# Optimization experiments

Measured on AMD Instinct MI355X. Metric: run time of the kernel, lower is better.

The kernel has to match this reference:

```python
import jax, jax.numpy as jnp
import numpy as np

# dims
B, S, D, H, DH, M, L, V, BS, NR = 4, 2048, 512, 8, 64, 2048, 6, 32000, 64, 3
NB = S // BS  # 32 blocks


def _block_plan(nb, seed):
    """BigBird block connectivity: 2 global + 3 window + NR random blocks per query block.
    Returns idx [nb, K] int32 and validity mask [nb, K] bool (dedup + edge handling)."""
    rng = np.random.RandomState(seed)
    K = 5 + NR
    idx = np.zeros((nb, K), np.int32)
    msk = np.zeros((nb, K), bool)
    for i in range(nb):
        fixed = {0, nb - 1} | {j for j in (i - 1, i, i + 1) if 0 <= j < nb}
        rest = [j for j in range(nb) if j not in fixed]
        rnd = rng.choice(rest, size=min(NR, len(rest)), replace=False) if rest else []
        sel = sorted(fixed | set(int(r) for r in rnd))
        idx[i, :len(sel)] = sel
        msk[i, :len(sel)] = True
    return jnp.asarray(idx), jnp.asarray(msk)


def _posemb():
    pos = np.arange(S, dtype=np.float32)[:, None]
    div = np.exp(np.arange(0, D, 2, dtype=np.float32) * (-np.log(10000.0) / D))
    pe = np.zeros((S, D), np.float32)
    pe[:, 0::2] = np.sin(pos * div)
    pe[:, 1::2] = np.cos(pos * div)
    return jnp.asarray(pe)


def _ln(x, scale, bias):
    m = jnp.mean(x, axis=-1, keepdims=True)
    v = jnp.mean(jnp.square(x - m), axis=-1, keepdims=True)
    return (x - m) * jax.lax.rsqrt(v + 1e-6) * scale + bias


def _bigbird_attn(x, key_mask, wq, wk, wv, wo, idx, bmask):
    # x: [B,S,D]; idx/bmask: [NB,K]
    q = jnp.einsum('bsd,dhe->bshe', x, wq).reshape(B, NB, BS, H, DH)
    k = jnp.einsum('bsd,dhe->bshe', x, wk).reshape(B, NB, BS, H, DH)
    v = jnp.einsum('bsd,dhe->bshe', x, wv).reshape(B, NB, BS, H, DH)
    kg = k[:, idx]  # [B,NB,K,BS,H,DH] gathered key blocks
    vg = v[:, idx]
    scores = jnp.einsum('bnqhe,bnkche->bhnqkc', q, kg) / jnp.sqrt(jnp.float32(DH))
    kmb = key_mask.reshape(B, NB, BS)[:, idx]          # [B,NB,K,BS]
    m = kmb & bmask[None, :, :, None]                   # [B,NB,K,BS]
    scores = jnp.where(m[:, None, :, None, :, :], scores, jnp.float32(-1e9))
    Kc = idx.shape[1]
    attn = jax.nn.softmax(scores.reshape(B, H, NB, BS, Kc * BS), axis=-1)
    attn = attn.reshape(B, H, NB, BS, Kc, BS)
    out = jnp.einsum('bhnqkc,bnkche->bnqhe', attn, vg).reshape(B, S, H, DH)
    return jnp.einsum('bshe,hed->bsd', out, wo)


def setup_inputs() -> dict:
    key = jax.random.key(0)
    ks = jax.random.split(key, 12)
    n = jax.random.normal
    inp = {
        'tokens': jax.random.randint(ks[0], (B, S), 0, V, dtype=jnp.int32),
        'embed': n(ks[1], (V, D), dtype=jnp.float32),
        'ln1_s': jnp.ones((L, D), jnp.float32), 'ln1_b': jnp.zeros((L, D), jnp.float32),
        'wq': n(ks[2], (L, D, H, DH), dtype=jnp.float32) * 0.02,
        'wk': n(ks[3], (L, D, H, DH), dtype=jnp.float32) * 0.02,
        'wv': n(ks[4], (L, D, H, DH), dtype=jnp.float32) * 0.02,
        'wo': n(ks[5], (L, H, DH, D), dtype=jnp.float32) * 0.02,
        'ln2_s': jnp.ones((L, D), jnp.float32), 'ln2_b': jnp.zeros((L, D), jnp.float32),
        'w1': n(ks[6], (L, D, M), dtype=jnp.float32) * 0.02, 'b1': jnp.zeros((L, M), jnp.float32),
        'w2': n(ks[7], (L, M, D), dtype=jnp.float32) * 0.02, 'b2': jnp.zeros((L, D), jnp.float32),
        'lnf_s': jnp.ones((D,), jnp.float32), 'lnf_b': jnp.zeros((D,), jnp.float32),
    }
    return inp


def reference(tokens, embed, ln1_s, ln1_b, wq, wk, wv, wo, ln2_s, ln2_b, w1, b1, w2, b2, lnf_s, lnf_b):
    key_mask = tokens > 0                      # src padding mask
    x = embed[tokens] + _posemb()[None]        # [B,S,D]
    plans = [_block_plan(NB, l) for l in range(L)]  # connectivity_seed = layer index
    for l in range(L):
        idx, bm = plans[l]
        h = _ln(x, ln1_s[l], ln1_b[l])
        x = x + _bigbird_attn(h, key_mask, wq[l], wk[l], wv[l], wo[l], idx, bm)
        y = _ln(x, ln2_s[l], ln2_b[l])
        y = jax.nn.gelu(jnp.einsum('bsd,dm->bsm', y, w1[l]) + b1[l])
        y = jnp.einsum('bsm,md->bsd', y, w2[l]) + b2[l]
        x = x + y
    return _ln(x, lnf_s, lnf_b)
```

## Files before the change

### kernel.cpp

```cpp
#include <hip/hip_runtime.h>

using u32 = unsigned int;
using u16 = unsigned short;

#define B_   4
#define S_   2048
#define D_   512
#define H_   8
#define DH_  64
#define FF_  2048
#define L_   6
#define NB_  32
#define KC_  8

typedef __attribute__((ext_vector_type(8))) __bf16 bf16x8;
typedef __attribute__((ext_vector_type(4))) float  f32x4;

struct Plan { unsigned char idx[NB_][KC_]; unsigned char cnt[NB_]; };

#define QSCALE 0.18033688011112042f

__device__ __forceinline__ u16 f2b(float f) {
  union { __bf16 b; u16 u; } x;
  x.b = (__bf16)f;
  return x.u;
}

__device__ __forceinline__ float gelu_f(float x) {
  float y2 = 1.5957691216f * x + 0.0713548163f * x * x * x;
  return x / (1.0f + __expf(-y2));
}

typedef const __attribute__((address_space(1))) u32* gas_t;
typedef __attribute__((address_space(3))) u32* las_t;
__device__ __forceinline__ void glds16(const u16* g, u16* l) {
  __builtin_amdgcn_global_load_lds((gas_t)g, (las_t)l, 16, 0, 0);
}

__global__ __launch_bounds__(256)
void transpose_conv(const float* __restrict__ in, u16* __restrict__ out, int R, int C,
                    size_t lstride, int rowoff) {
  __shared__ float tile[32][33];
  const int l = blockIdx.z;
  const float* src = in + (size_t)l * R * C;
  u16* dst = out + (size_t)l * lstride;
  const int c0 = blockIdx.x * 32, r0 = blockIdx.y * 32;
  const int tx = threadIdx.x, ty = threadIdx.y;
#pragma unroll
  for (int i = 0; i < 4; i++)
    tile[ty + i * 8][tx] = src[(size_t)(r0 + ty + i * 8) * C + c0 + tx];
  __syncthreads();
#pragma unroll
  for (int i = 0; i < 4; i++)
    dst[(size_t)(rowoff + c0 + ty + i * 8) * R + r0 + tx] = f2b(tile[tx][ty + i * 8]);
}

__global__ __launch_bounds__(128)
void embed_kernel(const int* __restrict__ tokens, const float* __restrict__ emb,
                  float* __restrict__ x) {
  const int row = blockIdx.x;
  const int s = row & (S_ - 1);
  const int t = threadIdx.x;
  const int tok = tokens[row];
  float4 v = ((const float4*)(emb + (size_t)tok * D_))[t];
  float va[4] = {v.x, v.y, v.z, v.w};
  const float cc = -2.0f * logf(10000.0f) / (float)D_;
  const float pos = (float)s;
#pragma unroll
  for (int j = 0; j < 4; j++) {
    int d = t * 4 + j;
    int i = d >> 1;
    float dv = expf(cc * (float)i);
    float ang = pos * dv;
    va[j] += (d & 1) ? cosf(ang) : sinf(ang);
  }
  ((float4*)x)[(size_t)row * (D_ / 4) + t] = make_float4(va[0], va[1], va[2], va[3]);
}

template <bool BF16OUT>
__global__ __launch_bounds__(128)
void ln_kernel(const float* __restrict__ x, const float* __restrict__ sc,
               const float* __restrict__ bi, void* __restrict__ outp) {
  const int row = blockIdx.x;
  const int t = threadIdx.x;
  float4 v = ((const float4*)(x + (size_t)row * D_))[t];
  float va[4] = {v.x, v.y, v.z, v.w};
  float s = va[0] + va[1] + va[2] + va[3];
  float sq = va[0] * va[0] + va[1] * va[1] + va[2] * va[2] + va[3] * va[3];
#pragma unroll
  for (int d = 1; d < 64; d <<= 1) {
    s  += __shfl_xor(s, d);
    sq += __shfl_xor(sq, d);
  }
  __shared__ float red[4];
  const int wv = t >> 6, lane = t & 63;
  if (lane == 0) { red[wv * 2] = s; red[wv * 2 + 1] = sq; }
  __syncthreads();
  const float ts  = red[0] + red[2];
  const float tsq = red[1] + red[3];
  const float mean = ts * (1.0f / (float)D_);
  const float inv  = rsqrtf(tsq * (1.0f / (float)D_) - mean * mean + 1e-6f);
  const int d0 = t * 4;
  float o[4];
#pragma unroll
  for (int j = 0; j < 4; j++)
    o[j] = (va[j] - mean) * inv * sc[d0 + j] + bi[d0 + j];
  if (BF16OUT) {
    ushort4 u;
    u.x = f2b(o[0]); u.y = f2b(o[1]); u.z = f2b(o[2]); u.w = f2b(o[3]);
    ((ushort4*)outp)[(size_t)row * (D_ / 4) + t] = u;
  } else {
    ((float4*)outp)[(size_t)row * (D_ / 4) + t] = make_float4(o[0], o[1], o[2], o[3]);
  }
}

template <int MODE, bool VSPLIT, int TM, int TN>
__global__ __launch_bounds__(TN * 2)
void gemm_pipe(const u16* __restrict__ A, const u16* __restrict__ BT,
               int Kk, int ostride, int ncols,
               float* __restrict__ outf, u16* __restrict__ outb,
               const float* __restrict__ bias, const float* __restrict__ resid,
               u16* __restrict__ vtout) {
  constexpr int NW  = TN / 32;
  constexpr int WC  = NW / 2;
  constexpr int MI  = TM / 32;
  constexpr int CHA = TM / (8 * NW);
  constexpr int CHB = TN / (8 * NW);
  constexpr int VM  = CHA + CHB;
  __shared__ u16 As[2][TM * 64];
  __shared__ u16 Bs[2][TN * 64];
  const int tid = threadIdx.x;
  const int wave = tid >> 6, lane = tid & 63;
  const int nwg = gridDim.x, cpx = nwg >> 3;
  const int bid = blockIdx.x;
  const int gid = (bid & 7) * cpx + (bid >> 3);
  const int row0 = (gid / ncols) * TM, col0 = (gid % ncols) * TN;
  const int wr = wave / WC, wc = wave % WC;
  const int l15 = lane & 15, l4 = lane >> 4;

  const u16* asrc[CHA];
  const u16* bsrc[CHB];
  int adst[CHA], bdst[CHB];
#pragma unroll
  for (int i = 0; i < CHA; i++) {
    int chunk = wave * (CHA * 64) + i * 64 + lane;
    int r = chunk >> 3, s = chunk & 7;
    asrc[i] = A + (size_t)(row0 + r) * Kk + ((s ^ (r & 7)) << 3);
    adst[i] = (wave * (CHA * 64) + i * 64) * 8;
  }
#pragma unroll
  for (int i = 0; i < CHB; i++) {
    int chunk = wave * (CHB * 64) + i * 64 + lane;
    int r = chunk >> 3, s = chunk & 7;
    bsrc[i] = BT + (size_t)(col0 + r) * Kk + ((s ^ (r & 7)) << 3);
    bdst[i] = (wave * (CHB * 64) + i * 64) * 8;
  }

  int aoff[MI], boff[4];
#pragma unroll
  for (int m = 0; m < MI; m++) aoff[m] = (wr * (MI * 16) + m * 16 + l15) * 64;
#pragma unroll
  for (int n = 0; n < 4; n++) boff[n] = (wc * 64 + n * 16 + l15) * 64;
  const int sk0 = ((l4)     ^ (l15 & 7)) << 3;
  const int sk1 = ((4 + l4) ^ (l15 & 7)) << 3;

  f32x4 acc[MI][4] = {};
  const int nk = Kk >> 6;

  auto stage = [&](int buf, int kt) {
    const int ko = kt << 6;
#pragma unroll
    for (int i = 0; i < CHA; i++) glds16(asrc[i] + ko, &As[buf][adst[i]]);
#pragma unroll
    for (int i = 0; i < CHB; i++) glds16(bsrc[i] + ko, &Bs[buf][bdst[i]]);
  };

  stage(0, 0);
  stage(1, 1);

  for (int kt = 0; kt < nk; ++kt) {
    const int cur = kt & 1;
    if (kt + 1 < nk) {
      if constexpr (VM == 8) { asm volatile("s_waitcnt vmcnt(8)" ::: "memory"); }
      else                   { asm volatile("s_waitcnt vmcnt(6)" ::: "memory"); }
    } else {
      asm volatile("s_waitcnt vmcnt(0)" ::: "memory");
    }
    __builtin_amdgcn_s_barrier();
    __builtin_amdgcn_sched_barrier(0);

    bf16x8 af0[MI], bf0[4];
#pragma unroll
    for (int m = 0; m < MI; m++) af0[m] = *(const bf16x8*)&As[cur][aoff[m] + sk0];
#pragma unroll
    for (int n = 0; n < 4; n++) bf0[n] = *(const bf16x8*)&Bs[cur][boff[n] + sk0];
#pragma unroll
    for (int m = 0; m < MI; m++)
#pragma unroll
      for (int n = 0; n < 4; n++)
        acc[m][n] = __builtin_amdgcn_mfma_f32_16x16x32_bf16(af0[m], bf0[n], acc[m][n], 0, 0, 0);

    bf16x8 af1[MI], bf1[4];
#pragma unroll
    for (int m = 0; m < MI; m++) af1[m] = *(const bf16x8*)&As[cur][aoff[m] + sk1];
#pragma unroll
    for (int n = 0; n < 4; n++) bf1[n] = *(const bf16x8*)&Bs[cur][boff[n] + sk1];
    asm volatile("s_waitcnt lgkmcnt(0)" ::: "memory");
    __builtin_amdgcn_sched_barrier(0);
    __builtin_amdgcn_s_barrier();
    __builtin_amdgcn_sched_barrier(0);
    if (kt + 2 < nk) stage(cur, kt + 2);

    __builtin_amdgcn_s_setprio(1);
#pragma unroll
    for (int m = 0; m < MI; m++)
#pragma unroll
      for (int n = 0; n < 4; n++)
        acc[m][n] = __builtin_amdgcn_mfma_f32_16x16x32_bf16(af1[m], bf1[n], acc[m][n], 0, 0, 0);
    __builtin_amdgcn_s_setprio(0);
  }

#pragma unroll
  for (int m = 0; m < MI; m++) {
#pragma unroll
    for (int n = 0; n < 4; n++) {
      const int c = col0 + wc * 64 + n * 16 + l15;
      const int rb = row0 + wr * (MI * 16) + m * 16 + l4 * 4;
      if (VSPLIT && c >= 1024) {
        u16 pk[4];
#pragma unroll
        for (int j = 0; j < 4; j++) pk[j] = f2b(acc[m][n][j]);
        *(uint2*)(vtout + (size_t)(c - 1024) * (B_ * S_) + rb) = *(const uint2*)pk;
      } else {
#pragma unroll
        for (int j = 0; j < 4; j++) {
          const size_t o = (size_t)(rb + j) * ostride + c;
          float v = acc[m][n][j];
          if (MODE == 0) {
            if (VSPLIT && c < 512) v *= QSCALE;
            outb[o] = f2b(v);
          } else if (MODE == 1) {
            outf[o] = v + resid[o];
          } else if (MODE == 2) {
            outb[o] = f2b(gelu_f(v + bias[c]));
          } else {
            outf[o] = v + bias[c] + resid[o];
          }
        }
      }
    }
  }
}

__global__ __launch_bounds__(256, 4)
void attn_mfma(const u16* __restrict__ qkv, const u16* __restrict__ vTg,
               const int* __restrict__ tokens, u16* __restrict__ outb, Plan plan) {
  __shared__ u16 ks[2][64 * 64];
  __shared__ u16 vt[2][64 * 64];
  __shared__ u16 ps[64 * 64];

  const int blk = blockIdx.x;
  const int h0 = blk & 7;
  const int n  = (blk >> 3) & 31;
  const int b  = blk >> 8;
  const int t  = threadIdx.x;
  const int wave = t >> 6, lane = t & 63;
  const int l15 = lane & 15, l4 = lane >> 4;
  const int ncnt = plan.cnt[n];
  const int qrow0 = b * S_ + n * 64;

  auto stage = [&](int bi, int c, int* tkd) {
    const int krow0 = b * S_ + c * 64;
#pragma unroll
    for (int i = 0; i < 2; i++) {
      int c0 = i * 256 + wave * 64;
      int cl = c0 + lane;
      int r = cl >> 3, s = cl & 7;
      int sw = (s ^ (r & 7)) << 3;
      glds16(qkv + (size_t)(krow0 + r) * 1024 + 512 + h0 * 64 + sw, &ks[bi][c0 * 8]);
      glds16(vTg + (size_t)(h0 * 64 + r) * (B_ * S_) + krow0 + sw, &vt[bi][c0 * 8]);
    }
#pragma unroll
    for (int nn = 0; nn < 4; nn++) tkd[nn] = tokens[krow0 + nn * 16 + l15];
  };

  bf16x8 qaf[2];
#pragma unroll
  for (int ks_ = 0; ks_ < 2; ks_++)
    qaf[ks_] = *(const bf16x8*)(qkv + (size_t)(qrow0 + wave * 16 + l15) * 1024 +
                                h0 * 64 + ks_ * 32 + l4 * 8);

  int tk[4], tn[4];
  stage(0, plan.idx[n][0], tk);

  f32x4 oacc[4] = {};
  float mrow[4], lrow[4];
#pragma unroll
  for (int j = 0; j < 4; j++) { mrow[j] = -3e38f; lrow[j] = 0.0f; }

  for (int kc = 0; kc < ncnt; kc++) {
    const int cur = kc & 1;
    __syncthreads();
    if (kc + 1 < ncnt) stage(cur ^ 1, plan.idx[n][kc + 1], tn);

    f32x4 sacc[4] = {};
#pragma unroll
    for (int nn = 0; nn < 4; nn++) {
      int r = nn * 16 + l15;
#pragma unroll
      for (int ks_ = 0; ks_ < 2; ks_++) {
        bf16x8 kf = *(const bf16x8*)(&ks[cur][r * 64 + ((ks_ * 32 + l4 * 8) ^ ((r & 7) << 3))]);
        sacc[nn] = __builtin_amdgcn_mfma_f32_16x16x32_bf16(qaf[ks_], kf, sacc[nn], 0, 0, 0);
      }
    }

    bool vld[4];
#pragma unroll
    for (int nn = 0; nn < 4; nn++) vld[nn] = tk[nn] > 0;

    float rmax[4];
#pragma unroll
    for (int j = 0; j < 4; j++) {
      float mj = -3e38f;
#pragma unroll
      for (int nn = 0; nn < 4; nn++)
        if (vld[nn]) mj = fmaxf(mj, sacc[nn][j]);
      rmax[j] = mj;
    }
#pragma unroll
    for (int d = 1; d < 16; d <<= 1) {
#pragma unroll
      for (int j = 0; j < 4; j++) rmax[j] = fmaxf(rmax[j], __shfl_xor(rmax[j], d));
    }
    int chg = 0;
#pragma unroll
    for (int j = 0; j < 4; j++) chg |= (rmax[j] > mrow[j]);
    if (__ballot(chg)) {
#pragma unroll
      for (int j = 0; j < 4; j++) {
        float mn = fmaxf(mrow[j], rmax[j]);
        float alpha = exp2f(mrow[j] - mn);
        mrow[j] = mn;
        lrow[j] *= alpha;
#pragma unroll
        for (int n2 = 0; n2 < 4; n2++) oacc[n2][j] *= alpha;
      }
    }
    float p[4][4];
#pragma unroll
    for (int j = 0; j < 4; j++) {
      float psum = 0.0f;
#pragma unroll
      for (int nn = 0; nn < 4; nn++) {
        float pv = vld[nn] ? exp2f(sacc[nn][j] - mrow[j]) : 0.0f;
        p[nn][j] = pv;
        psum += pv;
      }
      lrow[j] += psum;
    }

#pragma unroll
    for (int nn = 0; nn < 4; nn++)
#pragma unroll
      for (int j = 0; j < 4; j++) {
        int q = wave * 16 + l4 * 4 + j;
        ps[q * 64 + ((nn * 16 + l15) ^ ((q & 7) << 3))] = f2b(p[nn][j]);
      }

#pragma unroll
    for (int ks_ = 0; ks_ < 2; ks_++) {
      int r = wave * 16 + l15;
      bf16x8 paf = *(const bf16x8*)(ps + r * 64 + ((ks_ * 32 + l4 * 8) ^ ((r & 7) << 3)));
#pragma unroll
      for (int n2 = 0; n2 < 4; n2++) {
        int rv = n2 * 16 + l15;
        bf16x8 vf = *(const bf16x8*)(&vt[cur][rv * 64 + ((ks_ * 32 + l4 * 8) ^ ((rv & 7) << 3))]);
        oacc[n2] = __builtin_amdgcn_mfma_f32_16x16x32_bf16(paf, vf, oacc[n2], 0, 0, 0);
      }
    }
#pragma unroll
    for (int nn = 0; nn < 4; nn++) tk[nn] = tn[nn];
  }

#pragma unroll
  for (int d = 1; d < 16; d <<= 1) {
#pragma unroll
    for (int j = 0; j < 4; j++) lrow[j] += __shfl_xor(lrow[j], d);
  }
#pragma unroll
  for (int j = 0; j < 4; j++) {
    const float inv = lrow[j] > 0.0f ? 1.0f / lrow[j] : 0.0f;
    const int q = n * 64 + wave * 16 + l4 * 4 + j;
#pragma unroll
    for (int n2 = 0; n2 < 4; n2++) {
      outb[(size_t)(b * S_ + q) * D_ + h0 * 64 + n2 * 16 + l15] = f2b(oacc[n2][j] * inv);
    }
  }
}

namespace {
struct HostMT {
  u32 mt[624]; int mti;
  void seed(u32 s) {
    mt[0] = s;
    for (int i = 1; i < 624; i++)
      mt[i] = 1812433253u * (mt[i - 1] ^ (mt[i - 1] >> 30)) + (u32)i;
    mti = 624;
  }
  u32 next() {
    if (mti >= 624) {
      for (int k = 0; k < 624; k++) {
        u32 y = (mt[k] & 0x80000000u) | (mt[(k + 1) % 624] & 0x7fffffffu);
        mt[k] = mt[(k + 397) % 624] ^ (y >> 1) ^ ((y & 1u) ? 0x9908b0dfu : 0u);
      }
      mti = 0;
    }
    u32 y = mt[mti++];
    y ^= y >> 11;
    y ^= (y << 7)  & 0x9d2c5680u;
    y ^= (y << 15) & 0xefc60000u;
    y ^= y >> 18;
    return y;
  }
  u32 interval(u32 mx) {
    if (mx == 0u) return 0u;
    u32 mask = mx;
    mask |= mask >> 1; mask |= mask >> 2; mask |= mask >> 4;
    mask |= mask >> 8; mask |= mask >> 16;
    u32 v;
    while ((v = (next() & mask)) > mx) {}
    return v;
  }
};

void build_plan(int l, Plan* out) {
  HostMT rng;
  rng.seed((u32)l);
  for (int i = 0; i < NB_; i++) {
    bool fixedv[NB_] = {};
    fixedv[0] = true; fixedv[NB_ - 1] = true;
    for (int j = i - 1; j <= i + 1; j++)
      if (j >= 0 && j < NB_) fixedv[j] = true;
    int rest[NB_]; int nr = 0;
    for (int j = 0; j < NB_; j++) if (!fixedv[j]) rest[nr++] = j;
    int perm[NB_];
    for (int tt = 0; tt < nr; tt++) perm[tt] = tt;
    for (int tt = nr - 1; tt >= 1; tt--) {
      int j = (int)rng.interval((u32)tt);
      int tmp = perm[tt]; perm[tt] = perm[j]; perm[j] = tmp;
    }
    bool sel[NB_];
    for (int j = 0; j < NB_; j++) sel[j] = fixedv[j];
    for (int c = 0; c < 3; c++) sel[rest[perm[c]]] = true;
    int cnt = 0;
    for (int j = 0; j < NB_; j++)
      if (sel[j]) out->idx[i][cnt++] = (unsigned char)j;
    out->cnt[i] = (unsigned char)cnt;
    for (int c2 = cnt; c2 < KC_; c2++) out->idx[i][c2] = 0;
  }
}
}

extern "C" void kernel_launch(void* const* d_in, const int* in_sizes, int n_in,
                              void* d_out, int out_size, void* d_ws, size_t ws_size,
                              hipStream_t stream) {
  (void)in_sizes; (void)n_in; (void)out_size; (void)ws_size;

  const int*   tokens = (const int*)d_in[0];
  const float* embed  = (const float*)d_in[1];
  const float* ln1_s  = (const float*)d_in[2];
  const float* ln1_b  = (const float*)d_in[3];
  const float* wq     = (const float*)d_in[4];
  const float* wk     = (const float*)d_in[5];
  const float* wv     = (const float*)d_in[6];
  const float* wo     = (const float*)d_in[7];
  const float* ln2_s  = (const float*)d_in[8];
  const float* ln2_b  = (const float*)d_in[9];
  const float* w1     = (const float*)d_in[10];
  const float* b1     = (const float*)d_in[11];
  const float* w2     = (const float*)d_in[12];
  const float* b2     = (const float*)d_in[13];
  const float* lnf_s  = (const float*)d_in[14];
  const float* lnf_b  = (const float*)d_in[15];

  char* wp = (char*)d_ws;
  auto take = [&](size_t bytes) {
    void* p = (void*)wp;
    wp += (bytes + 255) & ~(size_t)255;
    return p;
  };

  const int Mrows = B_ * S_;
  u16* wqkvT = (u16*)take((size_t)L_ * 1536 * D_ * 2);
  u16* woT   = (u16*)take((size_t)L_ * D_ * D_ * 2);
  u16* w1T   = (u16*)take((size_t)L_ * FF_ * D_ * 2);
  u16* w2T   = (u16*)take((size_t)L_ * D_ * FF_ * 2);
  float* x   = (float*)take((size_t)Mrows * D_ * 4);
  u16* h     = (u16*)take((size_t)Mrows * D_ * 2);
  u16* big   = (u16*)take((size_t)Mrows * FF_ * 2);
  u16* qkv   = big;
  u16* vT    = big + (size_t)Mrows * 1024;
  u16* g     = big;

  Plan plans[L_];
  for (int l = 0; l < L_; l++) build_plan(l, &plans[l]);

  const size_t qkvL = (size_t)1536 * D_;

  transpose_conv<<<dim3(D_ / 32, D_ / 32, L_), dim3(32, 8), 0, stream>>>(wq, wqkvT, D_, D_, qkvL, 0);
  transpose_conv<<<dim3(D_ / 32, D_ / 32, L_), dim3(32, 8), 0, stream>>>(wk, wqkvT, D_, D_, qkvL, 512);
  transpose_conv<<<dim3(D_ / 32, D_ / 32, L_), dim3(32, 8), 0, stream>>>(wv, wqkvT, D_, D_, qkvL, 1024);
  transpose_conv<<<dim3(D_ / 32, D_ / 32, L_), dim3(32, 8), 0, stream>>>(wo, woT, D_, D_, (size_t)D_ * D_, 0);
  transpose_conv<<<dim3(FF_ / 32, D_ / 32, L_), dim3(32, 8), 0, stream>>>(w1, w1T, D_, FF_, (size_t)FF_ * D_, 0);
  transpose_conv<<<dim3(D_ / 32, FF_ / 32, L_), dim3(32, 8), 0, stream>>>(w2, w2T, FF_, D_, (size_t)D_ * FF_, 0);
  embed_kernel<<<Mrows, 128, 0, stream>>>(tokens, embed, x);

  for (int l = 0; l < L_; l++) {
    ln_kernel<true><<<Mrows, 128, 0, stream>>>(x, ln1_s + l * D_, ln1_b + l * D_, h);
    gemm_pipe<0, true, 128, 128><<<768, 256, 0, stream>>>(
        h, wqkvT + (size_t)l * qkvL, D_, 1024, 12, nullptr, qkv, nullptr, nullptr, vT);
    attn_mfma<<<B_ * NB_ * H_, 256, 0, stream>>>(qkv, vT, tokens, h, plans[l]);
    gemm_pipe<1, false, 64, 128><<<512, 256, 0, stream>>>(
        h, woT + (size_t)l * D_ * D_, D_, D_, 4, x, nullptr, nullptr, x, nullptr);
    ln_kernel<true><<<Mrows, 128, 0, stream>>>(x, ln2_s + l * D_, ln2_b + l * D_, h);
    gemm_pipe<2, false, 128, 128><<<1024, 256, 0, stream>>>(
        h, w1T + (size_t)l * FF_ * D_, D_, FF_, 16, nullptr, g, b1 + l * FF_, nullptr, nullptr);
    gemm_pipe<3, false, 64, 128><<<512, 256, 0, stream>>>(
        g, w2T + (size_t)l * D_ * FF_, FF_, D_, 4, x, nullptr, b2 + l * D_, x, nullptr);
  }
  ln_kernel<false><<<Mrows, 128, 0, stream>>>(x, lnf_s, lnf_b, d_out);
}
```

Before: 868.8 us.

## Fuse LayerNorm into output-projection and FFN-down GEMM epilogues and embedding

Drops the standalone LayerNorm kernels. LN1 of layer 0 now runs inside the embedding kernel. The Wo and W2 GEMMs are replaced by a new full-row GEMM (32 rows by all 512 columns per block) that adds bias and residual, writes x, and computes the next LayerNorm in its epilogue, with the final LN fused into the last layer. This saves kernel launches and one full read of x per LN, but the GEMM grid shrinks to 256 blocks of 512 threads with a narrow 32-row M tile, which may reduce B-tile reuse and occupancy.

```diff
diff --git a/kernel.cpp b/kernel.cpp
--- a/kernel.cpp
+++ b/kernel.cpp
@@ -56,8 +56,9 @@
 }
 
 __global__ __launch_bounds__(128)
-void embed_kernel(const int* __restrict__ tokens, const float* __restrict__ emb,
-                  float* __restrict__ x) {
+void embed_ln(const int* __restrict__ tokens, const float* __restrict__ emb,
+              const float* __restrict__ lns, const float* __restrict__ lnb,
+              float* __restrict__ x, u16* __restrict__ h) {
   const int row = blockIdx.x;
   const int s = row & (S_ - 1);
   const int t = threadIdx.x;
@@ -75,43 +76,29 @@
     va[j] += (d & 1) ? cosf(ang) : sinf(ang);
   }
   ((float4*)x)[(size_t)row * (D_ / 4) + t] = make_float4(va[0], va[1], va[2], va[3]);
-}
-
-template <bool BF16OUT>
-__global__ __launch_bounds__(128)
-void ln_kernel(const float* __restrict__ x, const float* __restrict__ sc,
-               const float* __restrict__ bi, void* __restrict__ outp) {
-  const int row = blockIdx.x;
-  const int t = threadIdx.x;
-  float4 v = ((const float4*)(x + (size_t)row * D_))[t];
-  float va[4] = {v.x, v.y, v.z, v.w};
-  float s = va[0] + va[1] + va[2] + va[3];
+
+  float sm = va[0] + va[1] + va[2] + va[3];
   float sq = va[0] * va[0] + va[1] * va[1] + va[2] * va[2] + va[3] * va[3];
 #pragma unroll
   for (int d = 1; d < 64; d <<= 1) {
-    s  += __shfl_xor(s, d);
+    sm += __shfl_xor(sm, d);
     sq += __shfl_xor(sq, d);
   }
   __shared__ float red[4];
   const int wv = t >> 6, lane = t & 63;
-  if (lane == 0) { red[wv * 2] = s; red[wv * 2 + 1] = sq; }
+  if (lane == 0) { red[wv * 2] = sm; red[wv * 2 + 1] = sq; }
   __syncthreads();
   const float ts  = red[0] + red[2];
   const float tsq = red[1] + red[3];
   const float mean = ts * (1.0f / (float)D_);
   const float inv  = rsqrtf(tsq * (1.0f / (float)D_) - mean * mean + 1e-6f);
   const int d0 = t * 4;
-  float o[4];
-#pragma unroll
-  for (int j = 0; j < 4; j++)
-    o[j] = (va[j] - mean) * inv * sc[d0 + j] + bi[d0 + j];
-  if (BF16OUT) {
-    ushort4 u;
-    u.x = f2b(o[0]); u.y = f2b(o[1]); u.z = f2b(o[2]); u.w = f2b(o[3]);
-    ((ushort4*)outp)[(size_t)row * (D_ / 4) + t] = u;
-  } else {
-    ((float4*)outp)[(size_t)row * (D_ / 4) + t] = make_float4(o[0], o[1], o[2], o[3]);
-  }
+  ushort4 u;
+  u.x = f2b((va[0] - mean) * inv * lns[d0 + 0] + lnb[d0 + 0]);
+  u.y = f2b((va[1] - mean) * inv * lns[d0 + 1] + lnb[d0 + 1]);
+  u.z = f2b((va[2] - mean) * inv * lns[d0 + 2] + lnb[d0 + 2]);
+  u.w = f2b((va[3] - mean) * inv * lns[d0 + 3] + lnb[d0 + 3]);
+  ((ushort4*)h)[(size_t)row * (D_ / 4) + t] = u;
 }
 
 template <int MODE, bool VSPLIT, int TM, int TN>
@@ -252,6 +239,155 @@
   }
 }
 
+template <bool HASBIAS, bool LAST>
+__global__ __launch_bounds__(512)
+void gemm_ln(const u16* __restrict__ A, const u16* __restrict__ BT, int Kk,
+             const float* __restrict__ bias, const float* __restrict__ resid,
+             float* __restrict__ xout, u16* __restrict__ hout,
+             float* __restrict__ dout,
+             const float* __restrict__ lns, const float* __restrict__ lnb) {
+  __shared__ u16 As[2][32 * 32];
+  __shared__ u16 Bs[2][512 * 32];
+  __shared__ float stats[32][8][2];
+  const int tid = threadIdx.x;
+  const int wave = tid >> 6, lane = tid & 63;
+  const int l15 = lane & 15, l4 = lane >> 4;
+  const int row0 = blockIdx.x * 32;
+
+  const u16* asrc = A;
+  int adst = 0;
+  if (wave < 2) {
+    int c = wave * 64 + lane;
+    int r = c >> 2, s = c & 3;
+    asrc = A + (size_t)(row0 + r) * Kk + ((s ^ (r & 3)) << 3);
+    adst = (wave * 64) * 8;
+  }
+  const u16* bsrc[4];
+  int bdst[4];
+#pragma unroll
+  for (int i = 0; i < 4; i++) {
+    int c = wave * 256 + i * 64 + lane;
+    int r = c >> 2, s = c & 3;
+    bsrc[i] = BT + (size_t)r * Kk + ((s ^ (r & 3)) << 3);
+    bdst[i] = (wave * 256 + i * 64) * 8;
+  }
+
+  int aoff[2], boff[4];
+#pragma unroll
+  for (int m = 0; m < 2; m++) aoff[m] = (m * 16 + l15) * 32 + ((l4 ^ (l15 & 3)) << 3);
+#pragma unroll
+  for (int n = 0; n < 4; n++) boff[n] = (wave * 64 + n * 16 + l15) * 32 + ((l4 ^ (l15 & 3)) << 3);
+
+  f32x4 acc[2][4] = {};
+  const int nk = Kk >> 5;
+
+  auto stage = [&](int buf, int kt) {
+    const int ko = kt << 5;
+    if (wave < 2) glds16(asrc + ko, &As[buf][adst]);
+#pragma unroll
+    for (int i = 0; i < 4; i++) glds16(bsrc[i] + ko, &Bs[buf][bdst[i]]);
+  };
+
+  stage(0, 0);
+
+  for (int kt = 0; kt < nk; ++kt) {
+    const int cur = kt & 1;
+    asm volatile("s_waitcnt vmcnt(0)" ::: "memory");
+    __builtin_amdgcn_s_barrier();
+    __builtin_amdgcn_sched_barrier(0);
+    if (kt + 1 < nk) stage(cur ^ 1, kt + 1);
+    bf16x8 af[2], bfr[4];
+#pragma unroll
+    for (int m = 0; m < 2; m++) af[m] = *(const bf16x8*)&As[cur][aoff[m]];
+#pragma unroll
+    for (int n = 0; n < 4; n++) bfr[n] = *(const bf16x8*)&Bs[cur][boff[n]];
+    asm volatile("s_waitcnt lgkmcnt(0)" ::: "memory");
+    __builtin_amdgcn_sched_barrier(0);
+    __builtin_amdgcn_s_setprio(1);
+#pragma unroll
+    for (int m = 0; m < 2; m++)
+#pragma unroll
+      for (int n = 0; n < 4; n++)
+        acc[m][n] = __builtin_amdgcn_mfma_f32_16x16x32_bf16(af[m], bfr[n], acc[m][n], 0, 0, 0);
+    __builtin_amdgcn_s_setprio(0);
+  }
+
+  float sum[2][4], sq[2][4];
+#pragma unroll
+  for (int m = 0; m < 2; m++)
+#pragma unroll
+    for (int j = 0; j < 4; j++) { sum[m][j] = 0.0f; sq[m][j] = 0.0f; }
+
+#pragma unroll
+  for (int m = 0; m < 2; m++) {
+#pragma unroll
+    for (int n = 0; n < 4; n++) {
+      const int c = wave * 64 + n * 16 + l15;
+      const float bv = HASBIAS ? bias[c] : 0.0f;
+#pragma unroll
+      for (int j = 0; j < 4; j++) {
+        const size_t o = (size_t)(row0 + m * 16 + l4 * 4 + j) * D_ + c;
+        float v = acc[m][n][j] + bv + resid[o];
+        acc[m][n][j] = v;
+        if (!LAST) xout[o] = v;
+        sum[m][j] += v;
+        sq[m][j] += v * v;
+      }
+    }
+  }
+#pragma unroll
+  for (int d = 1; d < 16; d <<= 1) {
+#pragma unroll
+    for (int m = 0; m < 2; m++)
+#pragma unroll
+      for (int j = 0; j < 4; j++) {
+        sum[m][j] += __shfl_xor(sum[m][j], d);
+        sq[m][j]  += __shfl_xor(sq[m][j], d);
+      }
+  }
+  if (l15 == 0) {
+#pragma unroll
+    for (int m = 0; m < 2; m++)
+#pragma unroll
+      for (int j = 0; j < 4; j++) {
+        const int r = m * 16 + l4 * 4 + j;
+        stats[r][wave][0] = sum[m][j];
+        stats[r][wave][1] = sq[m][j];
+      }
+  }
+  __syncthreads();
+
+  float mean[2][4], inv[2][4];
+#pragma unroll
+  for (int m = 0; m < 2; m++)
+#pragma unroll
+    for (int j = 0; j < 4; j++) {
+      const int r = m * 16 + l4 * 4 + j;
+      float s = 0.0f, q = 0.0f;
+#pragma unroll
+      for (int w = 0; w < 8; w++) { s += stats[r][w][0]; q += stats[r][w][1]; }
+      const float mn = s * (1.0f / (float)D_);
+      mean[m][j] = mn;
+      inv[m][j] = rsqrtf(q * (1.0f / (float)D_) - mn * mn + 1e-6f);
+    }
+
+#pragma unroll
+  for (int m = 0; m < 2; m++) {
+#pragma unroll
+    for (int n = 0; n < 4; n++) {
+      const int c = wave * 64 + n * 16 + l15;
+      const float g_ = lns[c], b_ = lnb[c];
+#pragma unroll
+      for (int j = 0; j < 4; j++) {
+        const size_t o = (size_t)(row0 + m * 16 + l4 * 4 + j) * D_ + c;
+        const float hv = (acc[m][n][j] - mean[m][j]) * inv[m][j] * g_ + b_;
+        if (LAST) dout[o] = hv;
+        else      hout[o] = f2b(hv);
+      }
+    }
+  }
+}
+
 __global__ __launch_bounds__(256, 4)
 void attn_mfma(const u16* __restrict__ qkv, const u16* __restrict__ vTg,
                const int* __restrict__ tokens, u16* __restrict__ outb, Plan plan) {
@@ -513,20 +649,25 @@
   transpose_conv<<<dim3(D_ / 32, D_ / 32, L_), dim3(32, 8), 0, stream>>>(wo, woT, D_, D_, (size_t)D_ * D_, 0);
   transpose_conv<<<dim3(FF_ / 32, D_ / 32, L_), dim3(32, 8), 0, stream>>>(w1, w1T, D_, FF_, (size_t)FF_ * D_, 0);
   transpose_conv<<<dim3(D_ / 32, FF_ / 32, L_), dim3(32, 8), 0, stream>>>(w2, w2T, FF_, D_, (size_t)D_ * FF_, 0);
-  embed_kernel<<<Mrows, 128, 0, stream>>>(tokens, embed, x);
+  embed_ln<<<Mrows, 128, 0, stream>>>(tokens, embed, ln1_s, ln1_b, x, h);
 
   for (int l = 0; l < L_; l++) {
-    ln_kernel<true><<<Mrows, 128, 0, stream>>>(x, ln1_s + l * D_, ln1_b + l * D_, h);
     gemm_pipe<0, true, 128, 128><<<768, 256, 0, stream>>>(
         h, wqkvT + (size_t)l * qkvL, D_, 1024, 12, nullptr, qkv, nullptr, nullptr, vT);
     attn_mfma<<<B_ * NB_ * H_, 256, 0, stream>>>(qkv, vT, tokens, h, plans[l]);
-    gemm_pipe<1, false, 64, 128><<<512, 256, 0, stream>>>(
-        h, woT + (size_t)l * D_ * D_, D_, D_, 4, x, nullptr, nullptr, x, nullptr);
-    ln_kernel<true><<<Mrows, 128, 0, stream>>>(x, ln2_s + l * D_, ln2_b + l * D_, h);
+    gemm_ln<false, false><<<Mrows / 32, 512, 0, stream>>>(
+        h, woT + (size_t)l * D_ * D_, D_, nullptr, x, x, h, nullptr,
+        ln2_s + l * D_, ln2_b + l * D_);
     gemm_pipe<2, false, 128, 128><<<1024, 256, 0, stream>>>(
         h, w1T + (size_t)l * FF_ * D_, D_, FF_, 16, nullptr, g, b1 + l * FF_, nullptr, nullptr);
-    gemm_pipe<3, false, 64, 128><<<512, 256, 0, stream>>>(
-        g, w2T + (size_t)l * D_ * FF_, FF_, D_, 4, x, nullptr, b2 + l * D_, x, nullptr);
-  }
-  ln_kernel<false><<<Mrows, 128, 0, stream>>>(x, lnf_s, lnf_b, d_out);
-}
+    if (l < L_ - 1) {
+      gemm_ln<true, false><<<Mrows / 32, 512, 0, stream>>>(
+          g, w2T + (size_t)l * D_ * FF_, FF_, b2 + l * D_, x, x, h, nullptr,
+          ln1_s + (l + 1) * D_, ln1_b + (l + 1) * D_);
+    } else {
+      gemm_ln<true, true><<<Mrows / 32, 512, 0, stream>>>(
+          g, w2T + (size_t)l * D_ * FF_, FF_, b2 + l * D_, x, nullptr, nullptr,
+          (float*)d_out, lnf_s, lnf_b);
+    }
+  }
+}
```

New measurement: 1.070 ms. 23.1% more time.
